# Performance work log

Measured on AMD Instinct MI355X. Metric: run time of the kernel, lower is better.

## Reference

```python
import jax, jax.numpy as jnp
import numpy as np

NUM_EMBEDDINGS = 50000
EMBEDDING_DIM = 1024
N_CENTROIDS = 256
BLOCK_SIZE = 8
N_BLOCKS = EMBEDDING_DIM // BLOCK_SIZE  # 128
BATCH, SEQ = 8, 2048


def setup_inputs() -> dict:
    key = jax.random.key(0)
    k1, k2, k3 = jax.random.split(key, 3)
    centroids = jax.random.normal(k1, (N_CENTROIDS, BLOCK_SIZE), dtype=jnp.float32)
    assignments = jax.random.randint(k2, (N_BLOCKS * NUM_EMBEDDINGS,), 0, N_CENTROIDS, dtype=jnp.int64)
    input_ids = jax.random.randint(k3, (BATCH, SEQ), 0, NUM_EMBEDDINGS, dtype=jnp.int64)
    return {"centroids": centroids, "assignments": assignments, "input_ids": input_ids}


def reference(centroids, assignments, input_ids):
    # Faithful to PQEmbedding.weight: gather centroids for every code,
    # reshape to [n_blocks, num_embeddings, block_size], permute to
    # [num_embeddings, n_blocks, block_size], flatten last two dims.
    weight = centroids[assignments]  # [n_blocks*num_embeddings, block_size]
    weight = weight.reshape(N_BLOCKS, NUM_EMBEDDINGS, BLOCK_SIZE)
    weight = jnp.transpose(weight, (1, 0, 2)).reshape(NUM_EMBEDDINGS, EMBEDDING_DIM)
    # Plain embedding lookup (padding_idx=None, max_norm=None)
    return weight[input_ids]  # [BATCH, SEQ, EMBEDDING_DIM]
```

## Files before the change

kernel.cpp:

```cpp
#include <hip/hip_runtime.h>

#define NUM_EMBEDDINGS 50000
#define EMBEDDING_DIM  1024
#define N_CENTROIDS    256
#define N_BLOCKS       128
#define N_TOKENS       16384
#define N_PARTS        8
#define BLKS_PER_PART  16
#define TOK_PER_BLOCK  64

typedef float f32x4 __attribute__((ext_vector_type(4)));

__global__ __launch_bounds__(256) void pq_embed_coop_kernel(
    const float* __restrict__ centroids,
    const int*   __restrict__ assignments,
    const int*   __restrict__ input_ids,
    float*       __restrict__ out)
{
    __shared__ int   ids_lds[TOK_PER_BLOCK];
    __shared__ int   codes_lds[TOK_PER_BLOCK * BLKS_PER_PART];
    __shared__ float c_lds[N_CENTROIDS * 9];

    const int tid  = threadIdx.x;
    const int part = blockIdx.x & (N_PARTS - 1);
    const int T0   = (blockIdx.x >> 3) * TOK_PER_BLOCK;

    {
        const f32x4* __restrict__ cg4 = reinterpret_cast<const f32x4*>(centroids);
        #pragma unroll
        for (int k = 0; k < 2; ++k) {
            const int i = tid + 256 * k;
            const f32x4 v = cg4[i];
            float* dst = &c_lds[(i >> 1) * 9 + (i & 1) * 4];
            dst[0] = v.x; dst[1] = v.y; dst[2] = v.z; dst[3] = v.w;
        }
    }
    if (tid < TOK_PER_BLOCK)
        ids_lds[tid] = input_ids[T0 + tid];
    __syncthreads();

    #pragma unroll
    for (int k = 0; k < 4; ++k) {
        const int p     = tid + 256 * k;
        const int tok   = p >> 4;
        const int blk16 = p & 15;
        const int id    = ids_lds[tok];
        codes_lds[p] = assignments[(size_t)(part * BLKS_PER_PART + blk16) * NUM_EMBEDDINGS + id];
    }
    __syncthreads();

    const int f4    = tid & 31;
    const int t8    = tid >> 5;
    const int blk16 = f4 >> 1;
    const int half  = f4 & 1;

    f32x4* __restrict__ o4 = reinterpret_cast<f32x4*>(out);

    #pragma unroll
    for (int k = 0; k < 8; ++k) {
        const int tok  = t8 + 8 * k;
        const int code = codes_lds[tok * BLKS_PER_PART + blk16];
        const float* __restrict__ cr = &c_lds[code * 9 + half * 4];
        f32x4 v;
        v.x = cr[0]; v.y = cr[1]; v.z = cr[2]; v.w = cr[3];
        __builtin_nontemporal_store(
            v, o4 + (size_t)(T0 + tok) * (EMBEDDING_DIM / 4) + part * 32 + f4);
    }
}

extern "C" void kernel_launch(void* const* d_in, const int* in_sizes, int n_in,
                              void* d_out, int out_size, void* d_ws, size_t ws_size,
                              hipStream_t stream) {
    const float* centroids   = (const float*)d_in[0];
    const int*   assignments = (const int*)d_in[1];
    const int*   input_ids   = (const int*)d_in[2];
    float*       out         = (float*)d_out;

    dim3 grid((N_TOKENS / TOK_PER_BLOCK) * N_PARTS);
    dim3 block(256);
    pq_embed_coop_kernel<<<grid, block, 0, stream>>>(centroids, assignments, input_ids, out);
}
```

Measured before the change: 20.13 us.

## Pipeline assignment-code gathers with output writes using double-buffered LDS chunks

```diff
diff --git a/kernel.cpp b/kernel.cpp
--- a/kernel.cpp
+++ b/kernel.cpp
@@ -8,22 +8,23 @@
 #define N_PARTS        8
 #define BLKS_PER_PART  16
 #define TOK_PER_BLOCK  64
+#define CHUNK          16
 
 typedef float f32x4 __attribute__((ext_vector_type(4)));
 
-__global__ __launch_bounds__(256) void pq_embed_coop_kernel(
+__global__ __launch_bounds__(256) void pq_embed_pipe_kernel(
     const float* __restrict__ centroids,
     const int*   __restrict__ assignments,
     const int*   __restrict__ input_ids,
     float*       __restrict__ out)
 {
     __shared__ int   ids_lds[TOK_PER_BLOCK];
-    __shared__ int   codes_lds[TOK_PER_BLOCK * BLKS_PER_PART];
+    __shared__ int   codes_lds[2][CHUNK * BLKS_PER_PART];
     __shared__ float c_lds[N_CENTROIDS * 9];
 
     const int tid  = threadIdx.x;
     const int part = blockIdx.x & (N_PARTS - 1);
-    const int T0   = (blockIdx.x >> 3) * TOK_PER_BLOCK;
+    const int TB   = (blockIdx.x >> 3) * TOK_PER_BLOCK;
 
     {
         const f32x4* __restrict__ cg4 = reinterpret_cast<const f32x4*>(centroids);
@@ -36,35 +37,41 @@
         }
     }
     if (tid < TOK_PER_BLOCK)
-        ids_lds[tid] = input_ids[T0 + tid];
+        ids_lds[tid] = input_ids[TB + tid];
     __syncthreads();
 
-    #pragma unroll
-    for (int k = 0; k < 4; ++k) {
-        const int p     = tid + 256 * k;
-        const int tok   = p >> 4;
-        const int blk16 = p & 15;
-        const int id    = ids_lds[tok];
-        codes_lds[p] = assignments[(size_t)(part * BLKS_PER_PART + blk16) * NUM_EMBEDDINGS + id];
-    }
-    __syncthreads();
+    const int tokp = tid >> 4;
+    const int blkp = tid & 15;
+    const int* __restrict__ arow =
+        assignments + (size_t)(part * BLKS_PER_PART + blkp) * NUM_EMBEDDINGS;
+
+    int creg = arow[ids_lds[tokp]];
 
     const int f4    = tid & 31;
-    const int t8    = tid >> 5;
+    const int t2    = tid >> 5;
     const int blk16 = f4 >> 1;
     const int half  = f4 & 1;
-
-    f32x4* __restrict__ o4 = reinterpret_cast<f32x4*>(out);
+    f32x4* __restrict__ o4 = reinterpret_cast<f32x4*>(out) + part * 32 + f4;
 
     #pragma unroll
-    for (int k = 0; k < 8; ++k) {
-        const int tok  = t8 + 8 * k;
-        const int code = codes_lds[tok * BLKS_PER_PART + blk16];
-        const float* __restrict__ cr = &c_lds[code * 9 + half * 4];
-        f32x4 v;
-        v.x = cr[0]; v.y = cr[1]; v.z = cr[2]; v.w = cr[3];
-        __builtin_nontemporal_store(
-            v, o4 + (size_t)(T0 + tok) * (EMBEDDING_DIM / 4) + part * 32 + f4);
+    for (int i = 0; i < 4; ++i) {
+        codes_lds[i & 1][tid] = creg;
+        __syncthreads();
+
+        if (i < 3)
+            creg = arow[ids_lds[CHUNK * (i + 1) + tokp]];
+
+        #pragma unroll
+        for (int s = 0; s < 2; ++s) {
+            const int tok  = t2 + 8 * s;
+            const int code = codes_lds[i & 1][tok * BLKS_PER_PART + blk16];
+            const float* __restrict__ cr = &c_lds[code * 9 + half * 4];
+            f32x4 v;
+            v.x = cr[0]; v.y = cr[1]; v.z = cr[2]; v.w = cr[3];
+            __builtin_nontemporal_store(
+                v, o4 + (size_t)(TB + CHUNK * i + tok) * (EMBEDDING_DIM / 4));
+        }
+        __syncthreads();
     }
 }
 
@@ -78,5 +85,5 @@
 
     dim3 grid((N_TOKENS / TOK_PER_BLOCK) * N_PARTS);
     dim3 block(256);
-    pq_embed_coop_kernel<<<grid, block, 0, stream>>>(centroids, assignments, input_ids, out);
+    pq_embed_pipe_kernel<<<grid, block, 0, stream>>>(centroids, assignments, input_ids, out);
 }
```

Measured after the change: 20.17 us. About the same (+0.2%).
